# Kernel tuning notes

Hardware: AMD Instinct MI355X
Metric: run time of the kernel (lower is better)

## Reference

```python
import jax, jax.numpy as jnp
import numpy as np

POINT_INFLUENCE = 1.0            # extent (sigma * grid_size)
KERNEL_RADIUS = 1.5 * POINT_INFLUENCE
N_KP = 15                        # n_kernel_points
DIM = 3
D_IN = 64
D_OUT = 64
N = 50000
M = 32
OFFSET_DIM = DIM * N_KP          # modulated=False


def setup_inputs() -> dict:
    key = jax.random.key(0)
    ks = jax.random.split(key, 8)
    query_points = jax.random.uniform(ks[0], (N, DIM), dtype=jnp.float32)
    support_points = jax.random.uniform(ks[1], (N, DIM), dtype=jnp.float32)
    neighbors = jax.random.randint(ks[2], (N, M), 0, N)
    x = jax.random.normal(ks[3], (N, D_IN), dtype=jnp.float32)
    # kernel point dispositions (load_kernels surrogate): center point fixed at 0,
    # remaining points inside the kernel ball of radius KERNEL_RADIUS
    kp = jax.random.uniform(ks[4], (N_KP, DIM), minval=-1.0, maxval=1.0, dtype=jnp.float32) * KERNEL_RADIUS
    K_points = kp.at[0].set(0.0)
    # xavier-normal-style params
    offset_weights = jax.random.normal(ks[5], (N_KP, D_IN, OFFSET_DIM), dtype=jnp.float32) * np.sqrt(2.0 / (D_IN + OFFSET_DIM))
    offset_bias = jnp.zeros((OFFSET_DIM,), dtype=jnp.float32)
    weight = jax.random.normal(ks[6], (N_KP, D_IN, D_OUT), dtype=jnp.float32) * np.sqrt(2.0 / (D_IN + D_OUT))
    return {
        "query_points": query_points,
        "support_points": support_points,
        "neighbors": neighbors,
        "x": x,
        "K_points": K_points,
        "offset_weights": offset_weights,
        "offset_bias": offset_bias,
        "weight": weight,
    }


def _kpconv_core(q, s, neigh, x, kpts, W, extent):
    """KPConv aggregation: kpts is [K,3] (rigid) or [N,K,3] (deformed)."""
    nb = s[neigh] - q[:, None, :]                          # [N,M,3] centered neighbors
    if kpts.ndim == 2:
        diff = nb[:, :, None, :] - kpts[None, None, :, :]  # [N,M,K,3]
    else:
        diff = nb[:, :, None, :] - kpts[:, None, :, :]     # [N,M,K,3]
    sqd = jnp.sum(diff * diff, axis=-1)                    # [N,M,K]
    # linear KP influence, aggregation_mode='sum'
    aw = jnp.maximum(1.0 - jnp.sqrt(sqd) / extent, 0.0)    # [N,M,K]
    aw = jnp.swapaxes(aw, 1, 2)                            # [N,K,M]
    nf = x[neigh]                                          # [N,M,Din]
    wf = jnp.einsum('nkm,nmd->nkd', aw, nf)                # [N,K,Din]
    return jnp.einsum('nkd,kde->ne', wf, W)                # [N,Dout]


def reference(query_points, support_points, neighbors, x, K_points, offset_weights, offset_bias, weight):
    # 1) rigid KPConv predicting per-query kernel-point offsets
    offset_feat = _kpconv_core(query_points, support_points, neighbors, x,
                               K_points, offset_weights, POINT_INFLUENCE) + offset_bias
    offsets = offset_feat.reshape(-1, N_KP, DIM) * POINT_INFLUENCE   # [N,K,3]
    # 2) deformable KPConv with per-query deformed kernel points
    deformed_K = K_points[None, :, :] + offsets                      # [N,K,3]
    new_feat = _kpconv_core(query_points, support_points, neighbors, x,
                            deformed_K, weight, POINT_INFLUENCE)
    return new_feat
```

## Files before the change

### kernel.cpp

```cpp
#include <hip/hip_runtime.h>

#define N_PTS 50000
#define M 32
#define KP 15
#define D 64
#define E1 45
#define P 16
#define WFS 1032

typedef __attribute__((ext_vector_type(8))) _Float16 f16x8;
typedef __attribute__((ext_vector_type(4))) float    f32x4;
typedef __attribute__((ext_vector_type(2))) _Float16 f16x2;
typedef __attribute__((ext_vector_type(2))) __fp16   fp16v2;

__device__ __forceinline__ unsigned pkrtz(float a, float b) {
    union { fp16v2 v; unsigned u; } x;
    x.v = __builtin_amdgcn_cvt_pkrtz(a, b);
    return x.u;
}
__device__ __forceinline__ unsigned pkrne(float a, float b) {
    union { f16x2 v; unsigned u; } x;
    x.v[0] = (_Float16)a; x.v[1] = (_Float16)b; return x.u;
}
__device__ __forceinline__ float h2f(unsigned bits16) {
    union { unsigned short s; _Float16 h; } x; x.s = (unsigned short)bits16;
    return (float)x.h;
}
__device__ __forceinline__ float fsqrt_fast(float x) {
#if __has_builtin(__builtin_amdgcn_sqrtf)
    return __builtin_amdgcn_sqrtf(x);
#else
    return sqrtf(x);
#endif
}
__device__ __forceinline__ void split2h(float a, float b, unsigned& hu, unsigned& lu) {
    hu = pkrtz(a, b);
    const float ra = a - h2f(hu & 0xffffu);
    const float rb = b - h2f(hu >> 16);
    lu = pkrtz(ra, rb);
}
__device__ __forceinline__ int aw_w(int k, int m) {
    return k * 32 + ((((m >> 3) ^ k) & 3) << 3) + (m & 7);
}
__device__ __forceinline__ int aw_r8(int row, int g) {
    return row * 32 + (((g ^ row) & 3) << 3);
}

#if defined(__HIP_DEVICE_COMPILE__) && __has_builtin(__builtin_amdgcn_perm)
__device__ __forceinline__ unsigned permb(unsigned a, unsigned b, unsigned sel) {
    return __builtin_amdgcn_perm(a, b, sel);
}
#else
__device__ __forceinline__ unsigned permb(unsigned a, unsigned b, unsigned sel) {
    if (sel == 0x05040100u) return (b & 0xffffu) | (a << 16);
    return (b >> 16) | (a & 0xffff0000u);
}
#endif

__global__ void prep_all(const float* __restrict__ x, const float* __restrict__ ow,
                         const float* __restrict__ w, unsigned* __restrict__ xw,
                         unsigned short* __restrict__ owh, unsigned short* __restrict__ owl,
                         unsigned short* __restrict__ wh)
{
    const int b = blockIdx.x, tid = threadIdx.x;
    if (b < 3125) {
        const int i = b * 256 + tid;
        const int n = i >> 4, c = i & 15;
        const float* src = x + n * 64 + c;
        uint2 u;
        u.x = pkrne(src[0],  src[16]);
        u.y = pkrne(src[32], src[48]);
        ((uint2*)xw)[i] = u;
    } else if (b < 3317) {
        const int t = (b - 3125) * 256 + tid;
        const int j = t & 7, lane = (t >> 3) & 63, rest = t >> 9;
        const int nt = rest % 3, ks = rest / 3;
        const int q = lane >> 4, c = lane & 15;
        const int pos  = ks * 32 + q * 8 + j;
        const int orig = pos ^ (((pos >> 6) & 3) << 2);
        const int d = orig >> 4, k = orig & 15, e = nt * 16 + c;
        const float v = (k < KP && e < E1) ? ow[k * (D * E1) + d * E1 + e] : 0.f;
        unsigned hu, lu; split2h(v, 0.f, hu, lu);
        owh[t] = (unsigned short)hu;
        owl[t] = (unsigned short)lu;
    } else {
        const int t = (b - 3317) * 256 + tid;
        const int j = t & 7, lane = (t >> 3) & 63, rest = t >> 9;
        const int nt = rest & 3, ks = rest >> 2;
        const int q = lane >> 4, c = lane & 15;
        const int pos = ks * 32 + q * 8 + j;
        const int k = pos >> 6, dsw = pos & 63;
        const int d = dsw ^ ((k & 7) << 3);
        const int e = nt * 16 + c;
        union { _Float16 h; unsigned short s; } cv;
        cv.h = (_Float16)w[k * (D * D) + d * D + e];
        wh[t] = cv.s;
    }
}

__global__ __launch_bounds__(512, 6) void kpconv_deform(
    const float* __restrict__ qpts, const float* __restrict__ spts,
    const int*   __restrict__ nbrs, const float* __restrict__ kpts,
    const float* __restrict__ obias,
    const unsigned* __restrict__ xw,
    const unsigned short* __restrict__ owh, const unsigned short* __restrict__ owl,
    const unsigned short* __restrict__ wh,
    float* __restrict__ out)
{
    __shared__ __align__(16) unsigned short s_nbr[P][M];
    __shared__ float s_q[P][3];
    __shared__ float s_off[P][E1];
    __shared__ __align__(16) unsigned short s_wfh[P][WFS];
    __shared__ __align__(16) unsigned short s_awB[P * 512];
    float (*s_part3)[16][49] = (float(*)[16][49])s_wfh;
    float (*s_red)[16][16]   = (float(*)[16][16])s_awB;

    const int tid  = threadIdx.x;
    const int base = blockIdx.x * P;
    const int lane = tid & 63;
    const int wid  = tid >> 6;
    const int q    = lane >> 4, c = lane & 15;
    const int pg   = tid >> 5, mg = tid & 31;

    float nbx, nby, nbz;
    f16x8 fbh[2][4];

    if (tid < P * 3)  ((float*)s_q)[tid]  = qpts[base * 3 + tid];
    __syncthreads();

    {
        const int ni = nbrs[(base + pg) * M + mg];
        s_nbr[pg][mg] = (unsigned short)ni;
        nbx = spts[ni * 3 + 0] - s_q[pg][0];
        nby = spts[ni * 3 + 1] - s_q[pg][1];
        nbz = spts[ni * 3 + 2] - s_q[pg][2];
        float av[16];
        av[15] = 0.f;
#pragma unroll
        for (int k = 0; k < KP; k++) {
            const float dx = nbx - kpts[k * 3 + 0];
            const float dy = nby - kpts[k * 3 + 1];
            const float dz = nbz - kpts[k * 3 + 2];
            av[k] = fmaxf(1.0f - fsqrt_fast(dx * dx + dy * dy + dz * dz), 0.f);
        }
        const int awp = pg * 512;
#pragma unroll
        for (int k2 = 0; k2 < 16; k2 += 2) {
            const unsigned hu = pkrne(av[k2], av[k2 + 1]);
            s_awB[awp + aw_w(k2, mg)]     = (unsigned short)hu;
            s_awB[awp + aw_w(k2 + 1, mg)] = (unsigned short)(hu >> 16);
        }
    }

    {
        const int hc = c >> 2;
        const uint2* __restrict__ xwq = (const uint2*)xw;
#pragma unroll
        for (int pi = 0; pi < 2; pi++) {
            const int p = 2 * wid + pi;
            const f16x8 ah = *(const f16x8*)&s_awB[p * 512 + aw_r8(lane & 15, q)];
            uint2 g2[8];
#pragma unroll
            for (int j = 0; j < 8; j++)
                g2[j] = xwq[(int)s_nbr[p][q * 8 + j] * 16 + c];
#pragma unroll
            for (int t = 0; t < 4; t++) {
                union { f16x8 v; unsigned u[4]; } bh;
#pragma unroll
                for (int jj = 0; jj < 4; jj++) {
                    const unsigned ga = (t < 2) ? g2[2 * jj + 1].x : g2[2 * jj + 1].y;
                    const unsigned gb = (t < 2) ? g2[2 * jj].x     : g2[2 * jj].y;
                    bh.u[jj] = permb(ga, gb, (t & 1) ? 0x07060302u : 0x05040100u);
                }
                fbh[pi][t] = bh.v;
                f32x4 dacc = {0.f, 0.f, 0.f, 0.f};
                dacc = __builtin_amdgcn_mfma_f32_16x16x32_f16(ah, bh.v, dacc, 0, 0, 0);
                const unsigned u01 = pkrne(dacc[0], dacc[1]);
                const unsigned u23 = pkrne(dacc[2], dacc[3]);
                const int eb = (t * 16 + c) * 16 + 4 * (q ^ hc);
                *(uint2*)&s_wfh[p][eb] = make_uint2(u01, u23);
            }
        }
    }
    __syncthreads();

    {
        const int pr = lane & 15;
        f32x4 acc0 = {0,0,0,0}, acc1 = {0,0,0,0}, acc2 = {0,0,0,0};
#pragma unroll
        for (int s = 0; s < 4; s++) {
            const int ks = wid * 4 + s;
            const f16x8 ahh = *(const f16x8*)&s_wfh[pr][ks * 32 + q * 8];
#pragma unroll
            for (int nt = 0; nt < 3; nt++) {
                const int f = ((ks * 3 + nt) * 64 + lane) * 8;
                const f16x8 bh = *(const f16x8*)&owh[f];
                const f16x8 bl = *(const f16x8*)&owl[f];
                f32x4* acc = (nt == 0) ? &acc0 : (nt == 1) ? &acc1 : &acc2;
                *acc = __builtin_amdgcn_mfma_f32_16x16x32_f16(ahh, bh, *acc, 0, 0, 0);
                *acc = __builtin_amdgcn_mfma_f32_16x16x32_f16(ahh, bl, *acc, 0, 0, 0);
            }
        }
        __syncthreads();
#pragma unroll
        for (int r = 0; r < 4; r++) {
            s_part3[wid][4 * q + r][0 * 16 + c] = acc0[r];
            s_part3[wid][4 * q + r][1 * 16 + c] = acc1[r];
            s_part3[wid][4 * q + r][2 * 16 + c] = acc2[r];
        }
    }
    __syncthreads();

    for (int idx = tid; idx < P * E1; idx += 512) {
        const int p = idx / E1, e = idx % E1;
        float v = obias[e];
#pragma unroll
        for (int w8 = 0; w8 < 8; w8++)
            v += s_part3[w8][p][e];
        s_off[p][e] = v;
    }
    __syncthreads();

    {
        unsigned pmask = 0;
        float av[16];
        av[15] = 0.f;
#pragma unroll
        for (int k = 0; k < KP; k++) {
            const float kx = kpts[k * 3 + 0] + s_off[pg][3 * k + 0];
            const float ky = kpts[k * 3 + 1] + s_off[pg][3 * k + 1];
            const float kz = kpts[k * 3 + 2] + s_off[pg][3 * k + 2];
            const float dx = nbx - kx, dy = nby - ky, dz = nbz - kz;
            av[k] = fmaxf(1.0f - fsqrt_fast(dx * dx + dy * dy + dz * dz), 0.f);
            pmask |= (__ballot(av[k] > 0.f) ? 1u : 0u) << k;
        }
        const int awp = pg * 512;
#pragma unroll
        for (int k2 = 0; k2 < 16; k2 += 2) {
            const unsigned hu = pkrne(av[k2], av[k2 + 1]);
            s_awB[awp + aw_w(k2, mg)]     = (unsigned short)hu;
            s_awB[awp + aw_w(k2 + 1, mg)] = (unsigned short)(hu >> 16);
        }
        if (lane == 0) *(unsigned*)&s_wfh[wid][1024] = pmask;
    }

    {
#pragma unroll
        for (int pi = 0; pi < 2; pi++) {
            const int p = 2 * wid + pi;
            const f16x8 awh_f = *(const f16x8*)&s_awB[p * 512 + aw_r8(lane & 15, q)];
#pragma unroll
            for (int t = 0; t < 4; t++) {
                f32x4 dacc = {0.f, 0.f, 0.f, 0.f};
                dacc = __builtin_amdgcn_mfma_f32_16x16x32_f16(fbh[pi][t], awh_f, dacc, 0, 0, 0);
                const unsigned u01 = pkrne(dacc[0], dacc[1]);
                const unsigned u23 = pkrne(dacc[2], dacc[3]);
                const int dsw = (t * 16 + 4 * q) ^ ((c & 7) << 3);
                *(uint2*)&s_wfh[p][c * 64 + dsw] = make_uint2(u01, u23);
            }
        }
    }
    __syncthreads();

    unsigned u2 = 0;
#pragma unroll
    for (int w = 0; w < 8; w++) u2 |= *(const unsigned*)&s_wfh[w][1024];

    {
        const int etile = wid & 3, kh = wid >> 2;
        const int pr = lane & 15;
        f32x4 acc = {0.f, 0.f, 0.f, 0.f};
#pragma unroll
        for (int k = 0; k < KP; k++) {
            if (!((u2 >> k) & 1)) continue;
            const int ks = k * 2 + kh;
            const f16x8 ah = *(const f16x8*)&s_wfh[pr][ks * 32 + q * 8];
            const f16x8 bh = *(const f16x8*)&wh[((ks * 4 + etile) * 64 + lane) * 8];
            acc = __builtin_amdgcn_mfma_f32_16x16x32_f16(ah, bh, acc, 0, 0, 0);
        }
        if (kh == 1) {
#pragma unroll
            for (int r = 0; r < 4; r++)
                s_red[etile][4 * q + r][c] = acc[r];
        }
        __syncthreads();
        if (kh == 0) {
#pragma unroll
            for (int r = 0; r < 4; r++)
                out[(base + 4 * q + r) * D + etile * 16 + c] =
                    acc[r] + s_red[etile][4 * q + r][c];
        }
    }
}

extern "C" void kernel_launch(void* const* d_in, const int* in_sizes, int n_in,
                              void* d_out, int out_size, void* d_ws, size_t ws_size,
                              hipStream_t stream) {
    const float* q   = (const float*)d_in[0];
    const float* s   = (const float*)d_in[1];
    const int*   nb  = (const int*)  d_in[2];
    const float* x   = (const float*)d_in[3];
    const float* kp  = (const float*)d_in[4];
    const float* ow  = (const float*)d_in[5];
    const float* ob  = (const float*)d_in[6];
    const float* w   = (const float*)d_in[7];
    float* out = (float*)d_out;

    unsigned*       xw  = (unsigned*)d_ws;
    unsigned short* owh = (unsigned short*)((char*)d_ws + 12800000);
    unsigned short* owl = (unsigned short*)((char*)d_ws + 12898304);
    unsigned short* wh  = (unsigned short*)((char*)d_ws + 12996608);

    prep_all<<<3557, 256, 0, stream>>>(x, ow, w, xw, owh, owl, wh);
    kpconv_deform<<<N_PTS / P, 512, 0, stream>>>(q, s, nb, kp, ob,
                                                 xw, owh, owl, wh, out);
}
```

Baseline: 151.6 us.

## Alias attention-weight tile into feature buffer to cut LDS and raise occupancy

Drops the separate 16 KB swizzled attention-weight buffer and stores the per-point weights inside each point's row of the existing feature buffer, using a padded stride of 36 instead of the XOR swizzle. The neighbor, query and offset arrays are packed into one small misc region that also holds the reduction scratch. Together these shrink per-block shared memory so more blocks fit per CU, and the launch-bounds occupancy hint is raised from 6 to 8 to match. The costs are possible LDS bank conflicts from the padded layout, register pressure or spills under the tighter occupancy hint, and reliance on reads and writes to the aliased rows being correctly ordered.

Measured after the change: 161.0 us. +6.2%, slower.

```diff
diff --git a/kernel.cpp b/kernel.cpp
--- a/kernel.cpp
+++ b/kernel.cpp
@@ -7,6 +7,7 @@
 #define E1 45
 #define P 16
 #define WFS 1032
+#define AWR 36
 
 typedef __attribute__((ext_vector_type(8))) _Float16 f16x8;
 typedef __attribute__((ext_vector_type(4))) float    f32x4;
@@ -38,12 +39,6 @@
     const float ra = a - h2f(hu & 0xffffu);
     const float rb = b - h2f(hu >> 16);
     lu = pkrtz(ra, rb);
-}
-__device__ __forceinline__ int aw_w(int k, int m) {
-    return k * 32 + ((((m >> 3) ^ k) & 3) << 3) + (m & 7);
-}
-__device__ __forceinline__ int aw_r8(int row, int g) {
-    return row * 32 + (((g ^ row) & 3) << 3);
 }
 
 #if defined(__HIP_DEVICE_COMPILE__) && __has_builtin(__builtin_amdgcn_perm)
@@ -98,7 +93,7 @@
     }
 }
 
-__global__ __launch_bounds__(512, 6) void kpconv_deform(
+__global__ __launch_bounds__(512, 8) void kpconv_deform(
     const float* __restrict__ qpts, const float* __restrict__ spts,
     const int*   __restrict__ nbrs, const float* __restrict__ kpts,
     const float* __restrict__ obias,
@@ -107,13 +102,13 @@
     const unsigned short* __restrict__ wh,
     float* __restrict__ out)
 {
-    __shared__ __align__(16) unsigned short s_nbr[P][M];
-    __shared__ float s_q[P][3];
-    __shared__ float s_off[P][E1];
     __shared__ __align__(16) unsigned short s_wfh[P][WFS];
-    __shared__ __align__(16) unsigned short s_awB[P * 512];
+    __shared__ __align__(16) char s_misc[4096];
+    unsigned short (*s_nbr)[M] = (unsigned short(*)[M])s_misc;
+    float (*s_q)[3]    = (float(*)[3])(s_misc + 1024);
+    float (*s_off)[E1] = (float(*)[E1])(s_misc + 1216);
     float (*s_part3)[16][49] = (float(*)[16][49])s_wfh;
-    float (*s_red)[16][16]   = (float(*)[16][16])s_awB;
+    float (*s_red)[16][16]   = (float(*)[16][16])s_misc;
 
     const int tid  = threadIdx.x;
     const int base = blockIdx.x * P;
@@ -143,12 +138,12 @@
             const float dz = nbz - kpts[k * 3 + 2];
             av[k] = fmaxf(1.0f - fsqrt_fast(dx * dx + dy * dy + dz * dz), 0.f);
         }
-        const int awp = pg * 512;
+        unsigned short* awp = &s_wfh[pg][0];
 #pragma unroll
         for (int k2 = 0; k2 < 16; k2 += 2) {
             const unsigned hu = pkrne(av[k2], av[k2 + 1]);
-            s_awB[awp + aw_w(k2, mg)]     = (unsigned short)hu;
-            s_awB[awp + aw_w(k2 + 1, mg)] = (unsigned short)(hu >> 16);
+            awp[k2 * AWR + mg]       = (unsigned short)hu;
+            awp[(k2 + 1) * AWR + mg] = (unsigned short)(hu >> 16);
         }
     }
 
@@ -158,7 +153,7 @@
 #pragma unroll
         for (int pi = 0; pi < 2; pi++) {
             const int p = 2 * wid + pi;
-            const f16x8 ah = *(const f16x8*)&s_awB[p * 512 + aw_r8(lane & 15, q)];
+            const f16x8 ah = *(const f16x8*)&s_wfh[p][(lane & 15) * AWR + q * 8];
             uint2 g2[8];
 #pragma unroll
             for (int j = 0; j < 8; j++)
@@ -234,12 +229,12 @@
             av[k] = fmaxf(1.0f - fsqrt_fast(dx * dx + dy * dy + dz * dz), 0.f);
             pmask |= (__ballot(av[k] > 0.f) ? 1u : 0u) << k;
         }
-        const int awp = pg * 512;
+        unsigned short* awp = &s_wfh[pg][0];
 #pragma unroll
         for (int k2 = 0; k2 < 16; k2 += 2) {
             const unsigned hu = pkrne(av[k2], av[k2 + 1]);
-            s_awB[awp + aw_w(k2, mg)]     = (unsigned short)hu;
-            s_awB[awp + aw_w(k2 + 1, mg)] = (unsigned short)(hu >> 16);
+            awp[k2 * AWR + mg]       = (unsigned short)hu;
+            awp[(k2 + 1) * AWR + mg] = (unsigned short)(hu >> 16);
         }
         if (lane == 0) *(unsigned*)&s_wfh[wid][1024] = pmask;
     }
@@ -248,7 +243,7 @@
 #pragma unroll
         for (int pi = 0; pi < 2; pi++) {
             const int p = 2 * wid + pi;
-            const f16x8 awh_f = *(const f16x8*)&s_awB[p * 512 + aw_r8(lane & 15, q)];
+            const f16x8 awh_f = *(const f16x8*)&s_wfh[p][(lane & 15) * AWR + q * 8];
 #pragma unroll
             for (int t = 0; t < 4; t++) {
                 f32x4 dacc = {0.f, 0.f, 0.f, 0.f};
```
